# Kernel optimization log

Measured on AMD Instinct MI355X. Metric: run time of the kernel, lower is better.

Reference implementation:

```python
import jax, jax.numpy as jnp
import numpy as np

N_CODES, N_EDGES, EMB, N_C, NNZ = 4096, 8192, 128, 4, 65536
ADD_RATIO, TEMP = 0.1, 0.5
MASK_VAL = -1e9


def setup_inputs() -> dict:
    key = jax.random.key(0)
    k1, k2, k3, k4, k5 = jax.random.split(key, 5)
    X = jax.random.normal(k1, (N_CODES, EMB), jnp.float32)
    V = jax.random.randint(k2, (NNZ,), 0, N_CODES)
    E = jax.random.randint(k3, (NNZ,), 0, N_EDGES)
    # incidence matrix has 1s exactly at the (V, E) nonzero entries
    H = jnp.zeros((N_CODES, N_EDGES), jnp.float32).at[V, E].set(1.0)
    p = jnp.clip(jax.random.uniform(k4, (N_CODES, N_EDGES), jnp.float32), 0.05, 0.95)
    cos_weight = jax.random.normal(k5, (N_C, EMB), jnp.float32)
    return {"X": X, "H": H, "V": V, "E": E,
            "incident_mask_prob": p, "cos_weight": cos_weight}


def _l2norm(x):
    # F.normalize(x, p=2, dim=-1, eps=1e-6): x / max(||x||, eps)
    n = jnp.sqrt(jnp.sum(x * x, axis=-1, keepdims=True))
    return x / jnp.maximum(n, 1e-6)


def reference(X, H, V, E, incident_mask_prob, cos_weight):
    num_edges = H.shape[1]
    n_c = cos_weight.shape[0]
    # 1) edge embeddings: scatter-mean of incident code embeddings
    sums = jax.ops.segment_sum(X[V], E, num_segments=num_edges)      # (M, D)
    cnt = jax.ops.segment_sum(jnp.ones((V.shape[0],), X.dtype), E,
                              num_segments=num_edges)                 # (M,)
    eX = sums / jnp.maximum(cnt, 1.0)[:, None]
    # 2) multi-head cosine similarity, mean over heads
    node_m = _l2norm(X[:, None, :] * cos_weight[None])               # (N, h, D)
    edge_m = _l2norm(eX[:, None, :] * cos_weight[None])              # (M, h, D)
    S = jnp.einsum('nhd,mhd->nm', node_m, edge_m) / n_c              # (N, M)
    # mask out existing incidences
    S = S.at[V, E].set(MASK_VAL)
    # 3) global top-k new incidences (k is static)
    k = int(ADD_RATIO * V.shape[0])
    _, idx = jax.lax.top_k(S.reshape(-1), k)
    row = idx // num_edges
    col = idx % num_edges
    delta_H = jnp.zeros_like(H).at[row, col].set(1.0)
    enriched_H = H + delta_H
    # 4) RelaxedBernoulli(temperature, probs).rsample()
    u = jax.random.uniform(jax.random.key(42), H.shape, H.dtype,
                           minval=1e-6, maxval=1.0 - 1e-6)
    logits = (jnp.log(incident_mask_prob) - jnp.log1p(-incident_mask_prob)
              + jnp.log(u) - jnp.log1p(-u)) / TEMP
    incident_mask = jax.nn.sigmoid(logits)
    return enriched_H * incident_mask
```

## Files before the change

### kernel.cpp

```cpp
#include <hip/hip_runtime.h>
#include <math.h>

#define N_CODES 4096
#define N_EDGES 8192
#define EMB     128
#define NHEAD   4
#define NNZ     65536
#define K_TOP   6553
#define S_TOTAL 33554432
#define NBINS   8192
#define NREP    16
#define CAP2    131072
#define SLACK_BINS 12
#define TIE_CAP 1024

typedef _Float16 f16_t;
typedef __attribute__((ext_vector_type(8))) _Float16 f16x8;
typedef __attribute__((ext_vector_type(4))) float f32x4;

__device__ __forceinline__ unsigned rotl32(unsigned v, int r) {
  return (v << r) | (v >> (32 - r));
}

__device__ float jax_u42(unsigned pos) {
  const unsigned ks0 = 0u, ks1 = 42u, ks2 = 0x1BD11BDAu ^ 0u ^ 42u;
  unsigned x0 = 0u  + ks0;
  unsigned x1 = pos + ks1;
#define TFR(r) { x0 += x1; x1 = rotl32(x1, (r)); x1 ^= x0; }
  TFR(13) TFR(15) TFR(26) TFR(6)   x0 += ks1; x1 += ks2 + 1u;
  TFR(17) TFR(29) TFR(16) TFR(24)  x0 += ks2; x1 += ks0 + 2u;
  TFR(13) TFR(15) TFR(26) TFR(6)   x0 += ks0; x1 += ks1 + 3u;
  TFR(17) TFR(29) TFR(16) TFR(24)  x0 += ks1; x1 += ks2 + 4u;
  TFR(13) TFR(15) TFR(26) TFR(6)   x0 += ks2; x1 += ks0 + 5u;
#undef TFR
  unsigned bits = x0 ^ x1;
  unsigned fb = (bits >> 9) | 0x3f800000u;
  float f = __uint_as_float(fb) - 1.0f;
  const float minv = 1e-6f;
  const float maxv = (float)(1.0 - 1e-6);
  float u = f * (maxv - minv) + minv;
  return fmaxf(minv, u);
}

__device__ float mask_val(float p, unsigned pos) {
  float u = jax_u42(pos);
  float l = (logf(p) - log1pf(-p) + logf(u) - log1pf(-u)) * 2.0f;
  return 1.0f / (1.0f + expf(-l));
}

__device__ __forceinline__ unsigned long long f64key(double v) {
  long long b = __double_as_longlong(v);
  return (b < 0) ? ~(unsigned long long)b
                 : ((unsigned long long)b | 0x8000000000000000ULL);
}

__global__ void count_k(const int* __restrict__ E, int* __restrict__ cnt) {
  int i = blockIdx.x * blockDim.x + threadIdx.x;
  if (i < NNZ) atomicAdd(&cnt[E[i]], 1);
}

__global__ __launch_bounds__(1024) void scan_k(const int* __restrict__ cnt,
                                               int* __restrict__ offs) {
  __shared__ int part[1024];
  int t = threadIdx.x;
  int local[8]; int s = 0;
  for (int j = 0; j < 8; ++j) { local[j] = cnt[t * 8 + j]; s += local[j]; }
  part[t] = s; __syncthreads();
  int v = s;
  for (int o = 1; o < 1024; o <<= 1) {
    int add = (t >= o) ? part[t - o] : 0;
    __syncthreads();
    v += add; part[t] = v;
    __syncthreads();
  }
  int base = v - s;
  for (int j = 0; j < 8; ++j) { offs[t * 8 + j] = base; base += local[j]; }
}

__global__ void scatter_k(const int* __restrict__ E, const int* __restrict__ offs,
                          int* __restrict__ cursor, int* __restrict__ bucket) {
  int i = blockIdx.x * blockDim.x + threadIdx.x;
  if (i < NNZ) {
    int e = E[i];
    int p = atomicAdd(&cursor[e], 1);
    bucket[offs[e] + p] = i;
  }
}

__global__ __launch_bounds__(128) void edge_k(const float* __restrict__ X,
                                              const int* __restrict__ V,
                                              const int* __restrict__ cnt,
                                              const int* __restrict__ offs,
                                              int* __restrict__ bucket,
                                              const float* __restrict__ W,
                                              f16_t* __restrict__ B16) {
  __shared__ int lst[512];
  __shared__ float red[2];
  int m = blockIdx.x, t = threadIdx.x;
  int deg = cnt[m], off = offs[m];
  int n = min(deg, 512);
  for (int j = t; j < n; j += 128) lst[j] = bucket[off + j];
  __syncthreads();
  if (t == 0 && n > 1) {
    for (int a = 1; a < n; ++a) {
      int key = lst[a]; int b = a - 1;
      while (b >= 0 && lst[b] > key) { lst[b + 1] = lst[b]; --b; }
      lst[b + 1] = key;
    }
  }
  __syncthreads();
  for (int j = t; j < n; j += 128) bucket[off + j] = lst[j];
  float s = 0.f;
  for (int j = 0; j < n; ++j) s += X[(size_t)V[lst[j]] * EMB + t];
  float eXd = s / fmaxf((float)deg, 1.0f);
  int lane = t & 63, wv = t >> 6;
  for (int h = 0; h < NHEAD; ++h) {
    float wd = W[h * EMB + t];
    float val = eXd * wd;
    float ss = val * val;
    for (int o = 32; o > 0; o >>= 1) ss += __shfl_down(ss, o, 64);
    if (lane == 0) red[wv] = ss;
    __syncthreads();
    float nh = 1.0f / fmaxf(sqrtf(red[0] + red[1]), 1e-6f);
    B16[(size_t)m * (NHEAD * EMB) + h * EMB + t] = (f16_t)(eXd * wd * wd * nh);
    __syncthreads();
  }
}

__global__ __launch_bounds__(128) void node_k(const float* __restrict__ X,
                                              const float* __restrict__ W,
                                              f16_t* __restrict__ A16) {
  __shared__ float red[2];
  int nid = blockIdx.x, t = threadIdx.x;
  float xd = X[(size_t)nid * EMB + t];
  int lane = t & 63, wv = t >> 6;
  for (int h = 0; h < NHEAD; ++h) {
    float val = xd * W[h * EMB + t];
    float ss = val * val;
    for (int o = 32; o > 0; o >>= 1) ss += __shfl_down(ss, o, 64);
    if (lane == 0) red[wv] = ss;
    __syncthreads();
    float nh = 1.0f / fmaxf(sqrtf(red[0] + red[1]), 1e-6f);
    A16[(size_t)nid * (NHEAD * EMB) + h * EMB + t] = (f16_t)(xd * nh);
    __syncthreads();
  }
}

__global__ __launch_bounds__(256) void gemm_hist(const f16_t* __restrict__ A16,
                                                 const f16_t* __restrict__ B16,
                                                 unsigned* __restrict__ ghist) {
  __shared__ __align__(16) f16_t As[128 * 32];
  __shared__ __align__(16) f16_t Bs[128 * 32];
  __shared__ unsigned hh[NBINS];
  const int tid  = threadIdx.x;
  const int lane = tid & 63;
  const int wv   = tid >> 6;
  const int m0   = blockIdx.x * 128;
  const int n0   = blockIdx.y * 128;
  const int wr   = (wv >> 1) * 64;
  const int wc   = (wv & 1) * 64;
  const int frow = lane & 15;
  const int fg   = lane >> 4;
  const int sw   = (frow >> 1) & 3;
  const int fo   = ((fg ^ sw) << 3);

  for (int i = tid; i < NBINS; i += 256) hh[i] = 0;

  f32x4 acc[4][4];
#pragma unroll
  for (int i = 0; i < 4; ++i)
#pragma unroll
    for (int j = 0; j < 4; ++j) acc[i][j] = (f32x4){0.f, 0.f, 0.f, 0.f};

  for (int k0 = 0; k0 < 512; k0 += 32) {
    __syncthreads();
#pragma unroll
    for (int r = 0; r < 2; ++r) {
      int chunk = r * 256 + wv * 64 + lane;
      int row   = chunk >> 2;
      int cb    = ((chunk & 3) ^ ((chunk >> 3) & 3)) << 3;
      __builtin_amdgcn_global_load_lds(
          (const __attribute__((address_space(1))) void*)
              (A16 + ((size_t)(n0 + row) << 9) + k0 + cb),
          (__attribute__((address_space(3))) void*)
              (As + (size_t)(r * 256 + wv * 64) * 8),
          16, 0, 0);
      __builtin_amdgcn_global_load_lds(
          (const __attribute__((address_space(1))) void*)
              (B16 + ((size_t)(m0 + row) << 9) + k0 + cb),
          (__attribute__((address_space(3))) void*)
              (Bs + (size_t)(r * 256 + wv * 64) * 8),
          16, 0, 0);
    }
    __syncthreads();
    f16x8 a[4], b[4];
#pragma unroll
    for (int i = 0; i < 4; ++i)
      a[i] = *(const f16x8*)(As + (wr + i * 16 + frow) * 32 + fo);
#pragma unroll
    for (int j = 0; j < 4; ++j)
      b[j] = *(const f16x8*)(Bs + (wc + j * 16 + frow) * 32 + fo);
#pragma unroll
    for (int i = 0; i < 4; ++i)
#pragma unroll
      for (int j = 0; j < 4; ++j)
        acc[i][j] = __builtin_amdgcn_mfma_f32_16x16x32_f16(a[i], b[j], acc[i][j], 0, 0, 0);
  }
#pragma unroll
  for (int i = 0; i < 4; ++i)
#pragma unroll
    for (int j = 0; j < 4; ++j)
#pragma unroll
      for (int q = 0; q < 4; ++q) {
        float v = acc[i][j][q] * 0.25f;
        float bf = fminf(fmaxf((v + 1.0f) * 4096.0f, 0.0f), (float)(NBINS - 1));
        atomicAdd(&hh[(int)bf], 1u);
      }
  __syncthreads();
  unsigned* gh = ghist + (size_t)(blockIdx.x & (NREP - 1)) * NBINS;
  for (int i = tid; i < NBINS; i += 256) {
    unsigned c = hh[i];
    if (c) atomicAdd(&gh[i], c);
  }
}

__global__ __launch_bounds__(256) void corr_k(const f16_t* __restrict__ A16,
                                              const f16_t* __restrict__ B16,
                                              const int* __restrict__ V,
                                              const int* __restrict__ E,
                                              unsigned* __restrict__ ghist) {
  int wave = threadIdx.x >> 6, lane = threadIdx.x & 63;
  int j = blockIdx.x * 4 + wave;
  if (j >= NNZ) return;
  int n = V[j], m = E[j];
  f16x8 a = *(const f16x8*)(A16 + ((size_t)n << 9) + lane * 8);
  f16x8 b = *(const f16x8*)(B16 + ((size_t)m << 9) + lane * 8);
  float s = 0.f;
#pragma unroll
  for (int c = 0; c < 8; ++c) s += (float)a[c] * (float)b[c];
  for (int o = 32; o > 0; o >>= 1) s += __shfl_down(s, o, 64);
  if (lane == 0) {
    float v = s * 0.25f;
    float bf = fminf(fmaxf((v + 1.0f) * 4096.0f, 0.0f), (float)(NBINS - 1));
    atomicAdd(&ghist[(size_t)(j & (NREP - 1)) * NBINS + (int)bf], (unsigned)-1);
  }
}

__global__ __launch_bounds__(1024) void thresh_k(const unsigned* __restrict__ hist,
                                                 float* __restrict__ T_lo) {
  __shared__ int suff[1024];
  int t = threadIdx.x;
  const int G = NBINS / 1024;
  int b0 = t * G;
  int s = 0;
  for (int j = 0; j < G; ++j) {
    unsigned tb = 0;
    for (int r = 0; r < NREP; ++r) tb += hist[(size_t)r * NBINS + b0 + j];
    s += (int)tb;
  }
  int v = s;
  suff[t] = v; __syncthreads();
  for (int o = 1; o < 1024; o <<= 1) {
    int add = (t + o < 1024) ? suff[t + o] : 0;
    __syncthreads();
    v += add; suff[t] = v;
    __syncthreads();
  }
  int above = (t < 1023) ? suff[t + 1] : 0;
  if (above < K_TOP && suff[t] >= K_TOP) {
    int running = above;
    int B = b0;
    for (int b = b0 + G - 1; b >= b0; --b) {
      unsigned tb = 0;
      for (int r = 0; r < NREP; ++r) tb += hist[(size_t)r * NBINS + b];
      running += (int)tb;
      if (running >= K_TOP) { B = b; break; }
    }
    B = max(B, SLACK_BINS);
    *T_lo = (float)(B - SLACK_BINS) * (1.0f / 4096.0f) - 1.0f;
  }
}

__global__ __launch_bounds__(256) void gemm_collect(const f16_t* __restrict__ A16,
                                                    const f16_t* __restrict__ B16,
                                                    const float* __restrict__ T_lo_p,
                                                    const int* __restrict__ V,
                                                    const int* __restrict__ cnt,
                                                    const int* __restrict__ offs,
                                                    const int* __restrict__ bucket,
                                                    unsigned* __restrict__ counter,
                                                    int* __restrict__ ci) {
  __shared__ __align__(16) f16_t As[128 * 32];
  __shared__ __align__(16) f16_t Bs[128 * 32];
  const int tid  = threadIdx.x;
  const int lane = tid & 63;
  const int wv   = tid >> 6;
  const int m0   = blockIdx.x * 128;
  const int n0   = blockIdx.y * 128;
  const int wr   = (wv >> 1) * 64;
  const int wc   = (wv & 1) * 64;
  const int frow = lane & 15;
  const int fg   = lane >> 4;
  const int sw   = (frow >> 1) & 3;
  const int fo   = ((fg ^ sw) << 3);
  const float T  = *T_lo_p;

  f32x4 acc[4][4];
#pragma unroll
  for (int i = 0; i < 4; ++i)
#pragma unroll
    for (int j = 0; j < 4; ++j) acc[i][j] = (f32x4){0.f, 0.f, 0.f, 0.f};

  for (int k0 = 0; k0 < 512; k0 += 32) {
    __syncthreads();
#pragma unroll
    for (int r = 0; r < 2; ++r) {
      int chunk = r * 256 + wv * 64 + lane;
      int row   = chunk >> 2;
      int cb    = ((chunk & 3) ^ ((chunk >> 3) & 3)) << 3;
      __builtin_amdgcn_global_load_lds(
          (const __attribute__((address_space(1))) void*)
              (A16 + ((size_t)(n0 + row) << 9) + k0 + cb),
          (__attribute__((address_space(3))) void*)
              (As + (size_t)(r * 256 + wv * 64) * 8),
          16, 0, 0);
      __builtin_amdgcn_global_load_lds(
          (const __attribute__((address_space(1))) void*)
              (B16 + ((size_t)(m0 + row) << 9) + k0 + cb),
          (__attribute__((address_space(3))) void*)
              (Bs + (size_t)(r * 256 + wv * 64) * 8),
          16, 0, 0);
    }
    __syncthreads();
    f16x8 a[4], b[4];
#pragma unroll
    for (int i = 0; i < 4; ++i)
      a[i] = *(const f16x8*)(As + (wr + i * 16 + frow) * 32 + fo);
#pragma unroll
    for (int j = 0; j < 4; ++j)
      b[j] = *(const f16x8*)(Bs + (wc + j * 16 + frow) * 32 + fo);
#pragma unroll
    for (int i = 0; i < 4; ++i)
#pragma unroll
      for (int j = 0; j < 4; ++j)
        acc[i][j] = __builtin_amdgcn_mfma_f32_16x16x32_f16(a[i], b[j], acc[i][j], 0, 0, 0);
  }
#pragma unroll
  for (int i = 0; i < 4; ++i)
#pragma unroll
    for (int j = 0; j < 4; ++j)
#pragma unroll
      for (int q = 0; q < 4; ++q) {
        float v = acc[i][j][q] * 0.25f;
        if (v >= T) {
          int m   = m0 + wc + j * 16 + frow;
          int row = n0 + wr + i * 16 + fg * 4 + q;
          int deg = min(cnt[m], 512), off = offs[m];
          bool member = false;
          for (int u = 0; u < deg; ++u)
            if (V[bucket[off + u]] == row) { member = true; break; }
          if (!member) {
            unsigned p = atomicAdd(counter, 1u);
            if (p < CAP2) ci[p] = (row << 13) | m;
          }
        }
      }
}

__global__ __launch_bounds__(256) void rescore_k(const float* __restrict__ X,
                                                 const float* __restrict__ W,
                                                 const int* __restrict__ V,
                                                 const int* __restrict__ cnt,
                                                 const int* __restrict__ offs,
                                                 const int* __restrict__ bucket,
                                                 const int* __restrict__ ci,
                                                 const unsigned* __restrict__ counter,
                                                 unsigned long long* __restrict__ ckey) {
  int C = (int)min(*counter, (unsigned)CAP2);
  int wave = threadIdx.x >> 6, lane = threadIdx.x & 63;
  int j = blockIdx.x * 4 + wave;
  if (j >= C) return;
  int pos = ci[j];
  int n = pos >> 13;
  int m = pos & 8191;
  int deg = cnt[m], off = offs[m];
  int nmem = min(deg, 512);
  double e0 = 0.0, e1 = 0.0;
  for (int q = 0; q < nmem; ++q) {
    const float* xv = X + (size_t)V[bucket[off + q]] * EMB;
    e0 += (double)xv[lane];
    e1 += (double)xv[lane + 64];
  }
  double dd = fmax((double)deg, 1.0);
  e0 /= dd; e1 /= dd;
  const float* xr = X + (size_t)n * EMB;
  double x0 = (double)xr[lane], x1 = (double)xr[lane + 64];
  double s = 0.0;
  for (int h = 0; h < NHEAD; ++h) {
    const float* wr = W + h * EMB;
    double w0 = (double)wr[lane], w1 = (double)wr[lane + 64];
    double xw0 = x0 * w0, xw1 = x1 * w1;
    double ew0 = e0 * w0, ew1 = e1 * w1;
    double an = xw0 * xw0 + xw1 * xw1;
    double ae = ew0 * ew0 + ew1 * ew1;
    double dt = xw0 * ew0 + xw1 * ew1;
    for (int o = 32; o > 0; o >>= 1) {
      an += __shfl_down(an, o, 64);
      ae += __shfl_down(ae, o, 64);
      dt += __shfl_down(dt, o, 64);
    }
    if (lane == 0) {
      double Nn = fmax(sqrt(an), 1e-6);
      double Ne = fmax(sqrt(ae), 1e-6);
      s += dt / (Nn * Ne);
    }
  }
  if (lane == 0) ckey[j] = f64key(s * 0.25);
}

__global__ __launch_bounds__(1024) void kth_k(const unsigned long long* __restrict__ keys,
                                              const unsigned* __restrict__ counter,
                                              unsigned long long* __restrict__ thr) {
  __shared__ unsigned hist[256];
  __shared__ unsigned long long s_prefix;
  __shared__ unsigned s_kleft, s_cgreat;
  int C = (int)min(*counter, (unsigned)CAP2);
  if (threadIdx.x == 0) { s_prefix = 0ULL; s_kleft = K_TOP; s_cgreat = 0u; }
  __syncthreads();
  for (int level = 7; level >= 0; --level) {
    for (int i = threadIdx.x; i < 256; i += 1024) hist[i] = 0;
    __syncthreads();
    unsigned long long prefix = s_prefix;
    unsigned long long pmask = (level == 7) ? 0ULL : (~0ULL << ((level + 1) * 8));
    for (int i = threadIdx.x; i < C; i += 1024) {
      unsigned long long k = keys[i];
      if ((k & pmask) == prefix)
        atomicAdd(&hist[(unsigned)((k >> (level * 8)) & 0xFF)], 1u);
    }
    __syncthreads();
    if (threadIdx.x == 0) {
      unsigned cum = 0; int b = 0;
      for (int i = 255; i >= 0; --i) {
        if (cum + hist[i] >= s_kleft) { b = i; break; }
        cum += hist[i];
      }
      s_prefix |= ((unsigned long long)b << (level * 8));
      s_kleft  -= cum;
      s_cgreat += cum;
    }
    __syncthreads();
  }
  if (threadIdx.x == 0) { thr[0] = s_prefix; thr[1] = (unsigned long long)s_cgreat; }
}

__global__ void write_k(const unsigned long long* __restrict__ keys,
                        const int* __restrict__ ci,
                        const unsigned* __restrict__ counter,
                        const unsigned long long* __restrict__ thr,
                        const float* __restrict__ P, float* __restrict__ out,
                        int* __restrict__ tiebuf, unsigned* __restrict__ tiecnt) {
  int C = (int)min(*counter, (unsigned)CAP2);
  int j = blockIdx.x * blockDim.x + threadIdx.x;
  if (j >= C) return;
  unsigned long long k = keys[j];
  unsigned long long t = thr[0];
  if (k > t) {
    unsigned pos = (unsigned)ci[j];
    out[pos] = mask_val(P[pos], pos);
  } else if (k == t) {
    unsigned q = atomicAdd(tiecnt, 1u);
    if (q < TIE_CAP) tiebuf[q] = ci[j];
  }
}

__global__ __launch_bounds__(256) void tiefin_k(const int* __restrict__ tiebuf,
                                                const unsigned* __restrict__ tiecnt,
                                                const unsigned long long* __restrict__ thr,
                                                const float* __restrict__ P,
                                                float* __restrict__ out) {
  __shared__ int idx[TIE_CAP];
  int T = (int)min(*tiecnt, (unsigned)TIE_CAP);
  int need = K_TOP - (int)thr[1];
  if (need <= 0 || T == 0) return;
  for (int i = threadIdx.x; i < T; i += 256) idx[i] = tiebuf[i];
  __syncthreads();
  if (threadIdx.x == 0 && T > 1) {
    for (int a = 1; a < T; ++a) {
      int key = idx[a]; int b = a - 1;
      while (b >= 0 && idx[b] > key) { idx[b + 1] = idx[b]; --b; }
      idx[b + 1] = key;
    }
  }
  __syncthreads();
  int m = min(need, T);
  for (int i = threadIdx.x; i < m; i += 256) {
    unsigned pos = (unsigned)idx[i];
    out[pos] = mask_val(P[pos], pos);
  }
}

__global__ void scatterH_k(const int* __restrict__ V, const int* __restrict__ E,
                           const float* __restrict__ P, float* __restrict__ out) {
  int i = blockIdx.x * blockDim.x + threadIdx.x;
  if (i >= NNZ) return;
  unsigned pos = (unsigned)V[i] * (unsigned)N_EDGES + (unsigned)E[i];
  out[pos] = mask_val(P[pos], pos);
}

extern "C" void kernel_launch(void* const* d_in, const int* in_sizes, int n_in,
                              void* d_out, int out_size, void* d_ws, size_t ws_size,
                              hipStream_t stream) {
  const float* X = (const float*)d_in[0];
  const int*   V = (const int*)d_in[2];
  const int*   E = (const int*)d_in[3];
  const float* P = (const float*)d_in[4];
  const float* W = (const float*)d_in[5];
  float* OUT = (float*)d_out;

  char* w = (char*)d_ws;
  int*      cnt      = (int*)(w + 0);
  int*      offs     = (int*)(w + 32768);
  int*      cursor   = (int*)(w + 65536);
  int*      bucket   = (int*)(w + 98304);
  unsigned* counter  = (unsigned*)(w + 360448);
  float*    T_lo     = (float*)(w + 360452);
  unsigned* tiecnt   = (unsigned*)(w + 360456);
  unsigned long long* thr = (unsigned long long*)(w + 360464);
  int*      cand_idx = (int*)(w + 360704);
  unsigned* ghist    = (unsigned*)(w + 360704);
  unsigned long long* cand_key = (unsigned long long*)(w + 884992);
  int*      tiebuf   = (int*)(w + 1933568);
  f16_t*    A16      = (f16_t*)(w + 1937664);
  f16_t*    B16      = (f16_t*)(w + 6131968);

  hipMemsetAsync(cnt,     0, 32768, stream);
  hipMemsetAsync(cursor,  0, 32768, stream);
  hipMemsetAsync((void*)(w + 360448), 0, 64, stream);
  hipMemsetAsync(ghist,   0, (size_t)NREP * NBINS * 4, stream);
  hipMemsetAsync(d_out,   0, (size_t)S_TOTAL * 4, stream);

  count_k    <<<NNZ / 256, 256, 0, stream>>>(E, cnt);
  scan_k     <<<1, 1024, 0, stream>>>(cnt, offs);
  scatter_k  <<<NNZ / 256, 256, 0, stream>>>(E, offs, cursor, bucket);
  edge_k     <<<N_EDGES, 128, 0, stream>>>(X, V, cnt, offs, bucket, W, B16);
  node_k     <<<N_CODES, 128, 0, stream>>>(X, W, A16);
  gemm_hist  <<<dim3(N_EDGES / 128, N_CODES / 128), 256, 0, stream>>>(A16, B16, ghist);
  corr_k     <<<NNZ / 4, 256, 0, stream>>>(A16, B16, V, E, ghist);
  thresh_k   <<<1, 1024, 0, stream>>>(ghist, T_lo);
  gemm_collect<<<dim3(N_EDGES / 128, N_CODES / 128), 256, 0, stream>>>(
      A16, B16, T_lo, V, cnt, offs, bucket, counter, cand_idx);
  rescore_k  <<<CAP2 / 4, 256, 0, stream>>>(X, W, V, cnt, offs, bucket,
                                            cand_idx, counter, cand_key);
  kth_k      <<<1, 1024, 0, stream>>>(cand_key, counter, thr);
  write_k    <<<CAP2 / 256, 256, 0, stream>>>(cand_key, cand_idx, counter, thr,
                                              P, OUT, tiebuf, tiecnt);
  tiefin_k   <<<1, 256, 0, stream>>>(tiebuf, tiecnt, thr, P, OUT);
  scatterH_k <<<NNZ / 256, 256, 0, stream>>>(V, E, P, OUT);
}
```

Before: 620.4 us.

## Materialize fp16 score matrix once instead of recomputing GEMM for candidate collection

The second GEMM pass is replaced by storing the similarity matrix as fp16 into the upper half of the output buffer during the histogram GEMM. A streaming collect kernel then scans it against the threshold, and a mask kernel marks existing incidences with -inf, which removes the per-element membership search. The GEMM also drops LDS staging in favour of direct register loads with double buffering, and histogram binning now uses the fp16-rounded value. This costs a 64MB write and read of scores, and the output memset is moved after collection so the scratch area is not cleared too early.

Measured after the change: 656.8 us. +5.9%, slower.

```diff
diff --git a/kernel.cpp b/kernel.cpp
--- a/kernel.cpp
+++ b/kernel.cpp
@@ -146,11 +146,10 @@
   }
 }
 
-__global__ __launch_bounds__(256) void gemm_hist(const f16_t* __restrict__ A16,
+__global__ __launch_bounds__(256, 2) void gemm_k(const f16_t* __restrict__ A16,
                                                  const f16_t* __restrict__ B16,
+                                                 unsigned short* __restrict__ S16,
                                                  unsigned* __restrict__ ghist) {
-  __shared__ __align__(16) f16_t As[128 * 32];
-  __shared__ __align__(16) f16_t Bs[128 * 32];
   __shared__ unsigned hh[NBINS];
   const int tid  = threadIdx.x;
   const int lane = tid & 63;
@@ -161,10 +160,12 @@
   const int wc   = (wv & 1) * 64;
   const int frow = lane & 15;
   const int fg   = lane >> 4;
-  const int sw   = (frow >> 1) & 3;
-  const int fo   = ((fg ^ sw) << 3);
 
   for (int i = tid; i < NBINS; i += 256) hh[i] = 0;
+  __syncthreads();
+
+  const f16_t* pA = A16 + ((size_t)(n0 + wr + frow) << 9) + fg * 8;
+  const f16_t* pB = B16 + ((size_t)(m0 + wc + frow) << 9) + fg * 8;
 
   f32x4 acc[4][4];
 #pragma unroll
@@ -172,40 +173,31 @@
 #pragma unroll
     for (int j = 0; j < 4; ++j) acc[i][j] = (f32x4){0.f, 0.f, 0.f, 0.f};
 
-  for (int k0 = 0; k0 < 512; k0 += 32) {
-    __syncthreads();
-#pragma unroll
-    for (int r = 0; r < 2; ++r) {
-      int chunk = r * 256 + wv * 64 + lane;
-      int row   = chunk >> 2;
-      int cb    = ((chunk & 3) ^ ((chunk >> 3) & 3)) << 3;
-      __builtin_amdgcn_global_load_lds(
-          (const __attribute__((address_space(1))) void*)
-              (A16 + ((size_t)(n0 + row) << 9) + k0 + cb),
-          (__attribute__((address_space(3))) void*)
-              (As + (size_t)(r * 256 + wv * 64) * 8),
-          16, 0, 0);
-      __builtin_amdgcn_global_load_lds(
-          (const __attribute__((address_space(1))) void*)
-              (B16 + ((size_t)(m0 + row) << 9) + k0 + cb),
-          (__attribute__((address_space(3))) void*)
-              (Bs + (size_t)(r * 256 + wv * 64) * 8),
-          16, 0, 0);
-    }
-    __syncthreads();
-    f16x8 a[4], b[4];
-#pragma unroll
-    for (int i = 0; i < 4; ++i)
-      a[i] = *(const f16x8*)(As + (wr + i * 16 + frow) * 32 + fo);
-#pragma unroll
-    for (int j = 0; j < 4; ++j)
-      b[j] = *(const f16x8*)(Bs + (wc + j * 16 + frow) * 32 + fo);
-#pragma unroll
-    for (int i = 0; i < 4; ++i)
-#pragma unroll
-      for (int j = 0; j < 4; ++j)
-        acc[i][j] = __builtin_amdgcn_mfma_f32_16x16x32_f16(a[i], b[j], acc[i][j], 0, 0, 0);
-  }
+  f16x8 a0[4], b0[4], a1[4], b1[4];
+
+#define LOADF(da, db, ks)                                                   \
+  _Pragma("unroll") for (int i = 0; i < 4; ++i)                             \
+    da[i] = *(const f16x8*)(pA + (size_t)i * (16 * 512) + (ks) * 32);       \
+  _Pragma("unroll") for (int j = 0; j < 4; ++j)                             \
+    db[j] = *(const f16x8*)(pB + (size_t)j * (16 * 512) + (ks) * 32);
+
+#define MM(aa, bb)                                                          \
+  _Pragma("unroll") for (int i = 0; i < 4; ++i)                             \
+    _Pragma("unroll") for (int j = 0; j < 4; ++j)                           \
+      acc[i][j] = __builtin_amdgcn_mfma_f32_16x16x32_f16(aa[i], bb[j],      \
+                                                         acc[i][j], 0, 0, 0);
+
+  LOADF(a0, b0, 0)
+#pragma unroll
+  for (int t = 0; t < 16; t += 2) {
+    LOADF(a1, b1, t + 1)
+    MM(a0, b0)
+    if (t + 2 < 16) { LOADF(a0, b0, t + 2) }
+    MM(a1, b1)
+  }
+#undef LOADF
+#undef MM
+
 #pragma unroll
   for (int i = 0; i < 4; ++i)
 #pragma unroll
@@ -213,7 +205,12 @@
 #pragma unroll
       for (int q = 0; q < 4; ++q) {
         float v = acc[i][j][q] * 0.25f;
-        float bf = fminf(fmaxf((v + 1.0f) * 4096.0f, 0.0f), (float)(NBINS - 1));
+        f16_t h = (f16_t)v;
+        int row = n0 + wr + i * 16 + fg * 4 + q;
+        int col = m0 + wc + j * 16 + frow;
+        S16[(size_t)row * N_EDGES + col] = __builtin_bit_cast(unsigned short, h);
+        float hv = (float)h;
+        float bf = fminf(fmaxf((hv + 1.0f) * 4096.0f, 0.0f), (float)(NBINS - 1));
         atomicAdd(&hh[(int)bf], 1u);
       }
   __syncthreads();
@@ -222,6 +219,12 @@
     unsigned c = hh[i];
     if (c) atomicAdd(&gh[i], c);
   }
+}
+
+__global__ void maskset16_k(const int* __restrict__ V, const int* __restrict__ E,
+                            unsigned short* __restrict__ S16) {
+  int i = blockIdx.x * blockDim.x + threadIdx.x;
+  if (i < NNZ) S16[(size_t)V[i] * N_EDGES + E[i]] = 0xFC00u;
 }
 
 __global__ __launch_bounds__(256) void corr_k(const f16_t* __restrict__ A16,
@@ -240,8 +243,8 @@
   for (int c = 0; c < 8; ++c) s += (float)a[c] * (float)b[c];
   for (int o = 32; o > 0; o >>= 1) s += __shfl_down(s, o, 64);
   if (lane == 0) {
-    float v = s * 0.25f;
-    float bf = fminf(fmaxf((v + 1.0f) * 4096.0f, 0.0f), (float)(NBINS - 1));
+    float hv = (float)(f16_t)(s * 0.25f);
+    float bf = fminf(fmaxf((hv + 1.0f) * 4096.0f, 0.0f), (float)(NBINS - 1));
     atomicAdd(&ghist[(size_t)(j & (NREP - 1)) * NBINS + (int)bf], (unsigned)-1);
   }
 }
@@ -281,90 +284,22 @@
   }
 }
 
-__global__ __launch_bounds__(256) void gemm_collect(const f16_t* __restrict__ A16,
-                                                    const f16_t* __restrict__ B16,
-                                                    const float* __restrict__ T_lo_p,
-                                                    const int* __restrict__ V,
-                                                    const int* __restrict__ cnt,
-                                                    const int* __restrict__ offs,
-                                                    const int* __restrict__ bucket,
-                                                    unsigned* __restrict__ counter,
-                                                    int* __restrict__ ci) {
-  __shared__ __align__(16) f16_t As[128 * 32];
-  __shared__ __align__(16) f16_t Bs[128 * 32];
-  const int tid  = threadIdx.x;
-  const int lane = tid & 63;
-  const int wv   = tid >> 6;
-  const int m0   = blockIdx.x * 128;
-  const int n0   = blockIdx.y * 128;
-  const int wr   = (wv >> 1) * 64;
-  const int wc   = (wv & 1) * 64;
-  const int frow = lane & 15;
-  const int fg   = lane >> 4;
-  const int sw   = (frow >> 1) & 3;
-  const int fo   = ((fg ^ sw) << 3);
-  const float T  = *T_lo_p;
-
-  f32x4 acc[4][4];
-#pragma unroll
-  for (int i = 0; i < 4; ++i)
-#pragma unroll
-    for (int j = 0; j < 4; ++j) acc[i][j] = (f32x4){0.f, 0.f, 0.f, 0.f};
-
-  for (int k0 = 0; k0 < 512; k0 += 32) {
-    __syncthreads();
-#pragma unroll
-    for (int r = 0; r < 2; ++r) {
-      int chunk = r * 256 + wv * 64 + lane;
-      int row   = chunk >> 2;
-      int cb    = ((chunk & 3) ^ ((chunk >> 3) & 3)) << 3;
-      __builtin_amdgcn_global_load_lds(
-          (const __attribute__((address_space(1))) void*)
-              (A16 + ((size_t)(n0 + row) << 9) + k0 + cb),
-          (__attribute__((address_space(3))) void*)
-              (As + (size_t)(r * 256 + wv * 64) * 8),
-          16, 0, 0);
-      __builtin_amdgcn_global_load_lds(
-          (const __attribute__((address_space(1))) void*)
-              (B16 + ((size_t)(m0 + row) << 9) + k0 + cb),
-          (__attribute__((address_space(3))) void*)
-              (Bs + (size_t)(r * 256 + wv * 64) * 8),
-          16, 0, 0);
-    }
-    __syncthreads();
-    f16x8 a[4], b[4];
-#pragma unroll
-    for (int i = 0; i < 4; ++i)
-      a[i] = *(const f16x8*)(As + (wr + i * 16 + frow) * 32 + fo);
-#pragma unroll
-    for (int j = 0; j < 4; ++j)
-      b[j] = *(const f16x8*)(Bs + (wc + j * 16 + frow) * 32 + fo);
-#pragma unroll
-    for (int i = 0; i < 4; ++i)
-#pragma unroll
-      for (int j = 0; j < 4; ++j)
-        acc[i][j] = __builtin_amdgcn_mfma_f32_16x16x32_f16(a[i], b[j], acc[i][j], 0, 0, 0);
-  }
-#pragma unroll
-  for (int i = 0; i < 4; ++i)
-#pragma unroll
-    for (int j = 0; j < 4; ++j)
-#pragma unroll
-      for (int q = 0; q < 4; ++q) {
-        float v = acc[i][j][q] * 0.25f;
-        if (v >= T) {
-          int m   = m0 + wc + j * 16 + frow;
-          int row = n0 + wr + i * 16 + fg * 4 + q;
-          int deg = min(cnt[m], 512), off = offs[m];
-          bool member = false;
-          for (int u = 0; u < deg; ++u)
-            if (V[bucket[off + u]] == row) { member = true; break; }
-          if (!member) {
-            unsigned p = atomicAdd(counter, 1u);
-            if (p < CAP2) ci[p] = (row << 13) | m;
-          }
-        }
+__global__ __launch_bounds__(256) void collect16_k(const f16x8* __restrict__ S8,
+                                                   const float* __restrict__ T_lo_p,
+                                                   unsigned* __restrict__ counter,
+                                                   int* __restrict__ ci) {
+  float T = *T_lo_p;
+  int stride = gridDim.x * blockDim.x;
+  for (int i = blockIdx.x * blockDim.x + threadIdx.x; i < S_TOTAL / 8; i += stride) {
+    f16x8 h = S8[i];
+#pragma unroll
+    for (int c = 0; c < 8; ++c) {
+      if ((float)h[c] >= T) {
+        unsigned j = atomicAdd(counter, 1u);
+        if (j < CAP2) ci[j] = i * 8 + c;
       }
+    }
+  }
 }
 
 __global__ __launch_bounds__(256) void rescore_k(const float* __restrict__ X,
@@ -517,6 +452,8 @@
   const float* W = (const float*)d_in[5];
   float* OUT = (float*)d_out;
 
+  unsigned short* S16 = (unsigned short*)((char*)d_out + (size_t)S_TOTAL * 2);
+
   char* w = (char*)d_ws;
   int*      cnt      = (int*)(w + 0);
   int*      offs     = (int*)(w + 32768);
@@ -537,23 +474,23 @@
   hipMemsetAsync(cursor,  0, 32768, stream);
   hipMemsetAsync((void*)(w + 360448), 0, 64, stream);
   hipMemsetAsync(ghist,   0, (size_t)NREP * NBINS * 4, stream);
-  hipMemsetAsync(d_out,   0, (size_t)S_TOTAL * 4, stream);
-
-  count_k    <<<NNZ / 256, 256, 0, stream>>>(E, cnt);
-  scan_k     <<<1, 1024, 0, stream>>>(cnt, offs);
-  scatter_k  <<<NNZ / 256, 256, 0, stream>>>(E, offs, cursor, bucket);
-  edge_k     <<<N_EDGES, 128, 0, stream>>>(X, V, cnt, offs, bucket, W, B16);
-  node_k     <<<N_CODES, 128, 0, stream>>>(X, W, A16);
-  gemm_hist  <<<dim3(N_EDGES / 128, N_CODES / 128), 256, 0, stream>>>(A16, B16, ghist);
-  corr_k     <<<NNZ / 4, 256, 0, stream>>>(A16, B16, V, E, ghist);
-  thresh_k   <<<1, 1024, 0, stream>>>(ghist, T_lo);
-  gemm_collect<<<dim3(N_EDGES / 128, N_CODES / 128), 256, 0, stream>>>(
-      A16, B16, T_lo, V, cnt, offs, bucket, counter, cand_idx);
-  rescore_k  <<<CAP2 / 4, 256, 0, stream>>>(X, W, V, cnt, offs, bucket,
-                                            cand_idx, counter, cand_key);
-  kth_k      <<<1, 1024, 0, stream>>>(cand_key, counter, thr);
-  write_k    <<<CAP2 / 256, 256, 0, stream>>>(cand_key, cand_idx, counter, thr,
-                                              P, OUT, tiebuf, tiecnt);
-  tiefin_k   <<<1, 256, 0, stream>>>(tiebuf, tiecnt, thr, P, OUT);
-  scatterH_k <<<NNZ / 256, 256, 0, stream>>>(V, E, P, OUT);
-}
+
+  count_k     <<<NNZ / 256, 256, 0, stream>>>(E, cnt);
+  scan_k      <<<1, 1024, 0, stream>>>(cnt, offs);
+  scatter_k   <<<NNZ / 256, 256, 0, stream>>>(E, offs, cursor, bucket);
+  edge_k      <<<N_EDGES, 128, 0, stream>>>(X, V, cnt, offs, bucket, W, B16);
+  node_k      <<<N_CODES, 128, 0, stream>>>(X, W, A16);
+  gemm_k      <<<dim3(N_EDGES / 128, N_CODES / 128), 256, 0, stream>>>(A16, B16, S16, ghist);
+  maskset16_k <<<NNZ / 256, 256, 0, stream>>>(V, E, S16);
+  corr_k      <<<NNZ / 4, 256, 0, stream>>>(A16, B16, V, E, ghist);
+  thresh_k    <<<1, 1024, 0, stream>>>(ghist, T_lo);
+  collect16_k <<<2048, 256, 0, stream>>>((const f16x8*)S16, T_lo, counter, cand_idx);
+  rescore_k   <<<CAP2 / 4, 256, 0, stream>>>(X, W, V, cnt, offs, bucket,
+                                             cand_idx, counter, cand_key);
+  kth_k       <<<1, 1024, 0, stream>>>(cand_key, counter, thr);
+  hipMemsetAsync(d_out, 0, (size_t)S_TOTAL * 4, stream);
+  write_k     <<<CAP2 / 256, 256, 0, stream>>>(cand_key, cand_idx, counter, thr,
+                                               P, OUT, tiebuf, tiecnt);
+  tiefin_k    <<<1, 256, 0, stream>>>(tiebuf, tiecnt, thr, P, OUT);
+  scatterH_k  <<<NNZ / 256, 256, 0, stream>>>(V, E, P, OUT);
+}
```
